# Performance work log

Measured on AMD Instinct MI355X. Metric: run time of the kernel, lower is better.

The kernel has to match this reference:

```python
import jax, jax.numpy as jnp
import numpy as np

HIDDEN = 2048
NUM_HEADS = 16
HEAD_DIM = HIDDEN // NUM_HEADS  # 128
LATENT = HIDDEN // 8            # 256
ROPE_THETA = 100000.0


def setup_inputs() -> dict:
    key = jax.random.key(0)
    ks = jax.random.split(key, 7)
    s = 0.02
    x = jax.random.normal(ks[0], (4, 1024, HIDDEN), dtype=jnp.float32)
    # weights stored as [in, out] (transpose of torch nn.Linear.weight)
    w_q_down = jax.random.normal(ks[1], (HIDDEN, LATENT), dtype=jnp.float32) * s
    w_kv_down = jax.random.normal(ks[2], (HIDDEN, LATENT), dtype=jnp.float32) * s
    w_q_up = jax.random.normal(ks[3], (LATENT, HIDDEN), dtype=jnp.float32) * s
    w_k_up = jax.random.normal(ks[4], (LATENT, HIDDEN), dtype=jnp.float32) * s
    w_v_up = jax.random.normal(ks[5], (LATENT, HIDDEN), dtype=jnp.float32) * s
    w_o = jax.random.normal(ks[6], (HIDDEN, HIDDEN), dtype=jnp.float32) * s
    return {"x": x, "w_q_down": w_q_down, "w_kv_down": w_kv_down,
            "w_q_up": w_q_up, "w_k_up": w_k_up, "w_v_up": w_v_up, "w_o": w_o}


def _rope_cos_sin(seq_len, dtype):
    # Llama rotary: inv_freq over even dims, emb = concat(freqs, freqs)
    inv_freq = 1.0 / (ROPE_THETA ** (jnp.arange(0, HEAD_DIM, 2, dtype=jnp.float32) / HEAD_DIM))
    pos = jnp.arange(seq_len, dtype=jnp.float32)
    freqs = pos[:, None] * inv_freq[None, :]          # [S, D/2]
    emb = jnp.concatenate([freqs, freqs], axis=-1)    # [S, D]
    return jnp.cos(emb).astype(dtype), jnp.sin(emb).astype(dtype)


def _rotate_half(t):
    h = t.shape[-1] // 2
    return jnp.concatenate([-t[..., h:], t[..., :h]], axis=-1)


def reference(x, w_q_down, w_kv_down, w_q_up, w_k_up, w_v_up, w_o):
    B, S, H = x.shape
    q_latent = x @ w_q_down                 # [B,S,latent]
    kv_latent = x @ w_kv_down               # [B,S,latent]
    q = (q_latent @ w_q_up).reshape(B, S, NUM_HEADS, HEAD_DIM)
    k = (kv_latent @ w_k_up).reshape(B, S, NUM_HEADS, HEAD_DIM)
    v = (kv_latent @ w_v_up).reshape(B, S, NUM_HEADS, HEAD_DIM)

    cos, sin = _rope_cos_sin(S, x.dtype)    # [S,D]
    cos = cos[None, :, None, :]             # [1,S,1,D] (unsqueeze_dim=2)
    sin = sin[None, :, None, :]
    q = q * cos + _rotate_half(q) * sin
    k = k * cos + _rotate_half(k) * sin

    # [B,H,S,D]
    q = q.transpose(0, 2, 1, 3)
    k = k.transpose(0, 2, 1, 3)
    v = v.transpose(0, 2, 1, 3)

    scale = 1.0 / jnp.sqrt(jnp.asarray(HEAD_DIM, dtype=x.dtype))
    scores = jnp.einsum('bhqd,bhkd->bhqk', q, k) * scale
    causal = jnp.tril(jnp.ones((S, S), dtype=bool))
    scores = jnp.where(causal[None, None], scores, jnp.finfo(scores.dtype).min)
    probs = jax.nn.softmax(scores, axis=-1)
    attn = jnp.einsum('bhqk,bhkd->bhqd', probs, v)  # [B,H,S,D]
    attn = attn.transpose(0, 2, 1, 3).reshape(B, S, H)
    return attn @ w_o
```

## Files before the change

kernel.cpp:

```cpp
#include <hip/hip_runtime.h>
#include <hip/hip_bf16.h>

typedef unsigned short u16;
typedef unsigned int u32;
typedef __attribute__((ext_vector_type(8))) __bf16 bf16x8;
typedef __attribute__((ext_vector_type(4))) float f32x4;

#define HID 2048
#define NH 16
#define HD 128
#define LAT 256
#define BATCH 4
#define SEQ 1024

__device__ __forceinline__ u16 f2bf(float f) {
  union { float f; u32 u; } v; v.f = f;
  u32 r = v.u + 0x7fffu + ((v.u >> 16) & 1u);
  return (u16)(r >> 16);
}

typedef const __attribute__((address_space(1))) u32 as1_u32;
typedef __attribute__((address_space(3))) u32 as3_u32;

__device__ __forceinline__ void load_lds16(const void* g, void* l) {
  __builtin_amdgcn_global_load_lds((as1_u32*)g, (as3_u32*)l, 16, 0, 0);
}

template<int WM, int WN, int MR, int NR>
__device__ __forceinline__ void gemm_core(const u16* __restrict__ A, const u16* __restrict__ Bt,
    int K, int lda, int ldb, int arow0, int brow0, u16* As, u16* Bs, f32x4 acc[MR][NR]) {
  constexpr int BM = WM * MR * 16, BN = WN * NR * 16;
  constexpr int NW = WM * WN;
  constexpr int ACH = (BM * 32) / 512;
  constexpr int BCH = (BN * 32) / 512;
  const int tid = threadIdx.x;
  const int lane = tid & 63, wave = tid >> 6;
  const int wm = wave % WM, wn = wave / WM;
  const int fr = lane & 15, fq = lane >> 4;

  for (int kt = 0; kt < K; kt += 32) {
    __syncthreads();
    #pragma unroll
    for (int cc = 0; cc < ACH / NW; ++cc) {
      int c = wave + cc * NW;
      int r = c * 16 + (lane >> 2);
      int col = (lane & 3) * 8;
      load_lds16(&A[(size_t)(arow0 + r) * lda + kt + col], &As[c * 512]);
    }
    #pragma unroll
    for (int cc = 0; cc < BCH / NW; ++cc) {
      int c = wave + cc * NW;
      int r = c * 16 + (lane >> 2);
      int col = (lane & 3) * 8;
      load_lds16(&Bt[(size_t)(brow0 + r) * ldb + kt + col], &Bs[c * 512]);
    }
    asm volatile("s_waitcnt vmcnt(0)" ::: "memory");
    __syncthreads();
    bf16x8 af[MR], bfr[NR];
    #pragma unroll
    for (int m = 0; m < MR; ++m)
      af[m] = *(const bf16x8*)&As[(wm * MR * 16 + m * 16 + fr) * 32 + fq * 8];
    #pragma unroll
    for (int n = 0; n < NR; ++n)
      bfr[n] = *(const bf16x8*)&Bs[(wn * NR * 16 + n * 16 + fr) * 32 + fq * 8];
    #pragma unroll
    for (int m = 0; m < MR; ++m)
      #pragma unroll
      for (int n = 0; n < NR; ++n)
        acc[m][n] = __builtin_amdgcn_mfma_f32_16x16x32_bf16(af[m], bfr[n], acc[m][n], 0, 0, 0);
  }
}

__global__ void __launch_bounds__(256) k_cvt(const float* __restrict__ in, u16* __restrict__ o, int n4) {
  int i = blockIdx.x * blockDim.x + threadIdx.x;
  if (i < n4) {
    float4 v = ((const float4*)in)[i];
    union { u16 s[4]; uint2 u; } w;
    w.s[0] = f2bf(v.x); w.s[1] = f2bf(v.y); w.s[2] = f2bf(v.z); w.s[3] = f2bf(v.w);
    ((uint2*)o)[i] = w.u;
  }
}

__global__ void __launch_bounds__(256) k_transpose3(const float* __restrict__ in0,
    const float* __restrict__ in1, const float* __restrict__ in2,
    u16* __restrict__ o0, u16* __restrict__ o1, u16* __restrict__ o2, int R, int C) {
  __shared__ float t[32][33];
  const float* in = blockIdx.z == 0 ? in0 : (blockIdx.z == 1 ? in1 : in2);
  u16* o = blockIdx.z == 0 ? o0 : (blockIdx.z == 1 ? o1 : o2);
  int bx = blockIdx.x * 32, by = blockIdx.y * 32;
  int tx = threadIdx.x, ty = threadIdx.y;
  #pragma unroll
  for (int i = ty; i < 32; i += 8) t[i][tx] = in[(size_t)(by + i) * C + bx + tx];
  __syncthreads();
  #pragma unroll
  for (int i = ty; i < 32; i += 8) o[(size_t)(bx + i) * R + by + tx] = f2bf(t[tx][i]);
}

__global__ void __launch_bounds__(256) k_cossin(float* __restrict__ cosT, float* __restrict__ sinT) {
  int idx = blockIdx.x * 256 + threadIdx.x;
  int s = idx >> 6, d = idx & 63;
  float inv = powf(100000.0f, -(float)d / 64.0f);
  float a = (float)s * inv;
  cosT[idx] = cosf(a);
  sinT[idx] = sinf(a);
}

__global__ void __launch_bounds__(512, 2) k_down(const u16* __restrict__ xb, const u16* __restrict__ wqdT,
    const u16* __restrict__ wkvdT, u16* __restrict__ ql, u16* __restrict__ kvl) {
  __shared__ __align__(16) u16 As[2][128 * 128];
  __shared__ __align__(16) u16 Bs[2][64 * 128];
  const u16* Bt = blockIdx.z ? wkvdT : wqdT;
  u16* out = blockIdx.z ? kvl : ql;
  const int rb = blockIdx.x * 128, cb = blockIdx.y * 64;
  const int tid = threadIdx.x, lane = tid & 63, wave = tid >> 6;
  const int wm = wave & 3, wn = wave >> 2;
  const int fr = lane & 15, fq = lane >> 4;
  const char* Ab = (const char*)xb;
  const char* Bb = (const char*)Bt;
  f32x4 acc[2][2] = {};

  auto stage = [&](int buf, int s) {
    #pragma unroll
    for (int cc = 0; cc < 4; ++cc) {
      int c = wave * 4 + cc;
      int L = c * 1024 + lane * 16;
      int Ls = L ^ (((L >> 8) & 7) << 4);
      int r = Ls >> 8, colb = Ls & 255;
      load_lds16(Ab + (size_t)(rb + r) * 4096 + s * 256 + colb, (char*)As[buf] + c * 1024);
    }
    #pragma unroll
    for (int cc = 0; cc < 2; ++cc) {
      int c = wave * 2 + cc;
      int L = c * 1024 + lane * 16;
      int Ls = L ^ (((L >> 8) & 7) << 4);
      int r = Ls >> 8, colb = Ls & 255;
      load_lds16(Bb + (size_t)(cb + r) * 4096 + s * 256 + colb, (char*)Bs[buf] + c * 1024);
    }
  };

  stage(0, 0);
  int buf = 0;
  for (int s = 0; s < 16; ++s) {
    if (s + 1 < 16) {
      stage(buf ^ 1, s + 1);
      asm volatile("s_waitcnt vmcnt(6)" ::: "memory");
    } else {
      asm volatile("s_waitcnt vmcnt(0)" ::: "memory");
    }
    asm volatile("s_barrier" ::: "memory");

    #pragma unroll
    for (int kk = 0; kk < 4; ++kk) {
      bf16x8 af[2], bfr[2];
      #pragma unroll
      for (int m = 0; m < 2; ++m) {
        int r = wm * 32 + m * 16 + fr;
        af[m] = *(const bf16x8*)((const char*)As[buf] + ((r * 256 + kk * 64 + fq * 16) ^ ((r & 7) << 4)));
      }
      #pragma unroll
      for (int n = 0; n < 2; ++n) {
        int r = wn * 32 + n * 16 + fr;
        bfr[n] = *(const bf16x8*)((const char*)Bs[buf] + ((r * 256 + kk * 64 + fq * 16) ^ ((r & 7) << 4)));
      }
      #pragma unroll
      for (int m = 0; m < 2; ++m)
        #pragma unroll
        for (int n = 0; n < 2; ++n)
          acc[m][n] = __builtin_amdgcn_mfma_f32_16x16x32_bf16(af[m], bfr[n], acc[m][n], 0, 0, 0);
    }

    asm volatile("s_barrier" ::: "memory");
    buf ^= 1;
  }

  #pragma unroll
  for (int m = 0; m < 2; ++m)
    #pragma unroll
    for (int n = 0; n < 2; ++n)
      #pragma unroll
      for (int i = 0; i < 4; ++i)
        out[(size_t)(rb + wm * 32 + m * 16 + fq * 4 + i) * LAT + cb + wn * 32 + n * 16 + fr] =
            f2bf(acc[m][n][i]);
}

__global__ void __launch_bounds__(256) k_up(const u16* __restrict__ ql, const u16* __restrict__ kvl,
    const u16* __restrict__ wquT, const u16* __restrict__ wkuT, const u16* __restrict__ wvuT,
    u16* __restrict__ q, u16* __restrict__ k, u16* __restrict__ vt,
    const float* __restrict__ cosT, const float* __restrict__ sinT) {
  __shared__ __align__(16) u16 As[128 * 32];
  __shared__ __align__(16) u16 Bs[128 * 32];
  const int mode = blockIdx.z;
  const u16* A = (mode == 0) ? ql : kvl;
  const u16* Bt = (mode == 0) ? wquT : (mode == 1 ? wkuT : wvuT);
  const int rb = blockIdx.x * 128;
  const int h = blockIdx.y;
  f32x4 acc[2][8] = {};
  gemm_core<4, 1, 2, 8>(A, Bt, LAT, LAT, LAT, rb, h * HD, As, Bs, acc);
  const int lane = threadIdx.x & 63, wave = threadIdx.x >> 6;
  const int fr = lane & 15, fq = lane >> 4;
  if (mode == 2) {
    #pragma unroll
    for (int m = 0; m < 2; ++m)
      #pragma unroll
      for (int n = 0; n < 8; ++n)
        #pragma unroll
        for (int i = 0; i < 4; ++i) {
          int row = rb + wave * 32 + m * 16 + fq * 4 + i;
          int b = row >> 10, s = row & 1023;
          int sp = (s & ~63) | (((s >> 4) & 1) << 5) | (((s >> 3) & 1) << 4) |
                   (((s >> 2) & 1) << 3) | (((s >> 5) & 1) << 2) | (s & 3);
          vt[(size_t)((b * NH + h) * HD + n * 16 + fr) * SEQ + sp] = f2bf(acc[m][n][i]);
        }
  } else {
    u16* dst = (mode == 0) ? q : k;
    const float scale = (mode == 0) ? 0.08838834764831845f * 1.4426950408889634f : 1.0f;
    #pragma unroll
    for (int m = 0; m < 2; ++m)
      #pragma unroll
      for (int i = 0; i < 4; ++i) {
        int row = rb + wave * 32 + m * 16 + fq * 4 + i;
        int b = row >> 10, s = row & 1023;
        size_t base = (size_t)((b * NH + h) * SEQ + s) * HD;
        #pragma unroll
        for (int j = 0; j < 4; ++j) {
          int dlo = j * 16 + fr;
          float c = cosT[s * 64 + dlo], sn = sinT[s * 64 + dlo];
          float x1 = acc[m][j][i], x2 = acc[m][j + 4][i];
          dst[base + dlo] = f2bf((x1 * c - x2 * sn) * scale);
          dst[base + dlo + 64] = f2bf((x2 * c + x1 * sn) * scale);
        }
      }
  }
}

__global__ void __launch_bounds__(1024, 1) k_attn(const u16* __restrict__ Q, const u16* __restrict__ Kc,
    const u16* __restrict__ Vt, u16* __restrict__ O) {
  __shared__ __align__(16) u16 Ks[2][64 * 128];
  __shared__ __align__(16) u16 Vs[2][128 * 64];
  const int f = blockIdx.x;
  const int bh = (f & 7) * 8 + ((f >> 3) & 7);
  const int jp = f >> 6;
  const int jh = 7 - jp, jl = jp;
  const int h = bh & (NH - 1), b = bh >> 4;
  const int tid = threadIdx.x, lane = tid & 63, wave = tid >> 6;
  const int fr = lane & 15, fq = lane >> 4;
  const int qw = ((wave < 8) ? jh : jl) * 128 + (wave & 7) * 16;
  const size_t qkb = (size_t)bh * SEQ * HD;
  const char* Kbase = (const char*)Kc + qkb * 2;
  const char* Vbase = (const char*)Vt + (size_t)bh * HD * SEQ * 2;
  const int nkt = 2 * jh + 2;

  auto stage = [&](int buf, int kt) {
    int c = wave;
    int L = c * 1024 + lane * 16;
    int Lk = L ^ (((L >> 8) & 7) << 4);
    load_lds16(Kbase + (size_t)kt * 16384 + Lk, (char*)Ks[buf] + c * 1024);
    int Lv = L ^ (((L >> 7) & 7) << 4);
    int rv = Lv >> 7, colb = Lv & 127;
    load_lds16(Vbase + (size_t)rv * (SEQ * 2) + (size_t)kt * 128 + colb, (char*)Vs[buf] + c * 1024);
  };

  bf16x8 ones;
  #pragma unroll
  for (int z = 0; z < 8; ++z) ones[z] = (__bf16)1.0f;

  bf16x8 qf[4];
  #pragma unroll
  for (int c = 0; c < 4; ++c)
    qf[c] = *(const bf16x8*)&Q[qkb + (size_t)(qw + fr) * HD + c * 32 + fq * 8];

  f32x4 ao[8] = {};
  f32x4 lacc = {};

  stage(0, 0);

  int cur = 0;
  for (int t = 0; t < nkt; ++t) {
    if (t + 1 < nkt) {
      stage(cur ^ 1, t + 1);
      asm volatile("s_waitcnt vmcnt(2)" ::: "memory");
    } else {
      asm volatile("s_waitcnt vmcnt(0)" ::: "memory");
    }
    asm volatile("s_barrier" ::: "memory");

    const int k0 = t * 64;
    if (k0 <= qw + 15) {
      f32x4 sc[4] = {};
      __builtin_amdgcn_s_setprio(1);
      #pragma unroll
      for (int c = 0; c < 4; ++c)
        #pragma unroll
        for (int n = 0; n < 4; ++n) {
          int rr = n * 16 + fr;
          int off = (rr * 256 + c * 64 + fq * 16) ^ ((rr & 7) << 4);
          bf16x8 kf = *(const bf16x8*)((const char*)Ks[cur] + off);
          sc[n] = __builtin_amdgcn_mfma_f32_16x16x32_bf16(kf, qf[c], sc[n], 0, 0, 0);
        }
      __builtin_amdgcn_s_setprio(0);

      const bool needmask = (k0 + 63 > qw);
      const int qrow = qw + fr;
      float p[4][4];
      #pragma unroll
      for (int n = 0; n < 4; ++n)
        #pragma unroll
        for (int i = 0; i < 4; ++i) {
          float sv = sc[n][i];
          if (needmask) {
            int kg = k0 + n * 16 + fq * 4 + i;
            sv = (kg <= qrow) ? sv : -1e30f;
          }
          p[n][i] = exp2f(sv);
        }
      bf16x8 pa[2];
      #pragma unroll
      for (int kf = 0; kf < 2; ++kf) {
        union { bf16x8 v; u32 w[4]; } pu;
        asm("v_cvt_pk_bf16_f32 %0, %1, %2" : "=v"(pu.w[0]) : "v"(p[kf][0]), "v"(p[kf][1]));
        asm("v_cvt_pk_bf16_f32 %0, %1, %2" : "=v"(pu.w[1]) : "v"(p[kf][2]), "v"(p[kf][3]));
        asm("v_cvt_pk_bf16_f32 %0, %1, %2" : "=v"(pu.w[2]) : "v"(p[2 + kf][0]), "v"(p[2 + kf][1]));
        asm("v_cvt_pk_bf16_f32 %0, %1, %2" : "=v"(pu.w[3]) : "v"(p[2 + kf][2]), "v"(p[2 + kf][3]));
        pa[kf] = pu.v;
      }

      __builtin_amdgcn_s_setprio(1);
      lacc = __builtin_amdgcn_mfma_f32_16x16x32_bf16(pa[0], ones, lacc, 0, 0, 0);
      lacc = __builtin_amdgcn_mfma_f32_16x16x32_bf16(pa[1], ones, lacc, 0, 0, 0);
      #pragma unroll
      for (int jj = 0; jj < 8; ++jj)
        #pragma unroll
        for (int kf = 0; kf < 2; ++kf) {
          int rv = jj * 16 + fr;
          int off = (rv * 128 + kf * 64 + fq * 16) ^ ((rv & 7) << 4);
          bf16x8 vf = *(const bf16x8*)((const char*)Vs[cur] + off);
          ao[jj] = __builtin_amdgcn_mfma_f32_16x16x32_bf16(pa[kf], vf, ao[jj], 0, 0, 0);
        }
      __builtin_amdgcn_s_setprio(0);
    }
    asm volatile("s_barrier" ::: "memory");
    cur ^= 1;
  }

  #pragma unroll
  for (int i = 0; i < 4; ++i) {
    float inv = 1.f / lacc[i];
    int s = qw + fq * 4 + i;
    size_t base = (size_t)(b * SEQ + s) * HID + h * HD;
    #pragma unroll
    for (int jj = 0; jj < 8; ++jj)
      O[base + jj * 16 + fr] = f2bf(ao[jj][i] * inv);
  }
}

__global__ void __launch_bounds__(256) k_out(const u16* __restrict__ at, const u16* __restrict__ woT,
    float* __restrict__ out) {
  __shared__ __align__(16) u16 As[128 * 128];
  __shared__ __align__(16) u16 Bs[128 * 128];
  const int rb = blockIdx.x * 128, cb = blockIdx.y * 128;
  const int tid = threadIdx.x, lane = tid & 63, wave = tid >> 6;
  const int wm = wave & 1, wn = wave >> 1;
  const int fr = lane & 15, fq = lane >> 4;
  const char* Ab = (const char*)at;
  const char* Bb = (const char*)woT;

  f32x4 acc[4][4] = {};

  for (int kt = 0; kt < HID; kt += 128) {
    __syncthreads();
    #pragma unroll
    for (int cc = 0; cc < 8; ++cc) {
      int c = wave * 8 + cc;
      int L = c * 1024 + lane * 16;
      int Ls = L ^ (((L >> 8) & 7) << 4);
      int r = Ls >> 8, colb = Ls & 255;
      load_lds16(Ab + (size_t)(rb + r) * (HID * 2) + kt * 2 + colb, (char*)As + c * 1024);
      load_lds16(Bb + (size_t)(cb + r) * (HID * 2) + kt * 2 + colb, (char*)Bs + c * 1024);
    }
    asm volatile("s_waitcnt vmcnt(0)" ::: "memory");
    __syncthreads();

    #pragma unroll
    for (int kk = 0; kk < 4; ++kk) {
      bf16x8 af[4], bfr[4];
      #pragma unroll
      for (int m = 0; m < 4; ++m) {
        int r = wm * 64 + m * 16 + fr;
        af[m] = *(const bf16x8*)((const char*)As + ((r * 256 + kk * 64 + fq * 16) ^ ((r & 7) << 4)));
      }
      #pragma unroll
      for (int n = 0; n < 4; ++n) {
        int r = wn * 64 + n * 16 + fr;
        bfr[n] = *(const bf16x8*)((const char*)Bs + ((r * 256 + kk * 64 + fq * 16) ^ ((r & 7) << 4)));
      }
      #pragma unroll
      for (int m = 0; m < 4; ++m)
        #pragma unroll
        for (int n = 0; n < 4; ++n)
          acc[m][n] = __builtin_amdgcn_mfma_f32_16x16x32_bf16(af[m], bfr[n], acc[m][n], 0, 0, 0);
    }
  }

  #pragma unroll
  for (int m = 0; m < 4; ++m)
    #pragma unroll
    for (int n = 0; n < 4; ++n)
      #pragma unroll
      for (int i = 0; i < 4; ++i)
        out[(size_t)(rb + wm * 64 + m * 16 + fq * 4 + i) * HID + cb + wn * 64 + n * 16 + fr] =
            acc[m][n][i];
}

extern "C" void kernel_launch(void* const* d_in, const int* in_sizes, int n_in,
                              void* d_out, int out_size, void* d_ws, size_t ws_size,
                              hipStream_t stream) {
  const float* x    = (const float*)d_in[0];
  const float* wqd  = (const float*)d_in[1];
  const float* wkvd = (const float*)d_in[2];
  const float* wqu  = (const float*)d_in[3];
  const float* wku  = (const float*)d_in[4];
  const float* wvu  = (const float*)d_in[5];
  const float* wo   = (const float*)d_in[6];
  float* out = (float*)d_out;

  char* p = (char*)d_ws;
  u16* xb    = (u16*)(p + 0);
  u16* at    = xb;
  u16* wqdT  = (u16*)(p + 16777216);
  u16* wkvdT = (u16*)(p + 17825792);
  u16* wquT  = (u16*)(p + 18874368);
  u16* wkuT  = (u16*)(p + 19922944);
  u16* wvuT  = (u16*)(p + 20971520);
  u16* woT   = (u16*)(p + 22020096);
  u16* ql    = (u16*)(p + 30408704);
  u16* kvl   = (u16*)(p + 32505856);
  u16* q     = (u16*)(p + 34603008);
  u16* kk    = (u16*)(p + 51380224);
  u16* vt    = (u16*)(p + 68157440);
  float* cosT = (float*)(p + 84934656);
  float* sinT = (float*)(p + 85196800);

  k_cvt<<<8192, 256, 0, stream>>>(x, xb, 2097152);
  k_transpose3<<<dim3(8, 64, 2), dim3(32, 8), 0, stream>>>(wqd, wkvd, wkvd, wqdT, wkvdT, wkvdT, 2048, 256);
  k_transpose3<<<dim3(64, 8, 3), dim3(32, 8), 0, stream>>>(wqu, wku, wvu, wquT, wkuT, wvuT, 256, 2048);
  k_transpose3<<<dim3(64, 64, 1), dim3(32, 8), 0, stream>>>(wo, wo, wo, woT, woT, woT, 2048, 2048);
  k_cossin<<<256, 256, 0, stream>>>(cosT, sinT);

  k_down<<<dim3(32, 4, 2), 512, 0, stream>>>(xb, wqdT, wkvdT, ql, kvl);
  k_up<<<dim3(32, 16, 3), 256, 0, stream>>>(ql, kvl, wquT, wkuT, wvuT, q, kk, vt, cosT, sinT);
  k_attn<<<256, 1024, 0, stream>>>(q, kk, vt, at);
  k_out<<<dim3(32, 16), 256, 0, stream>>>(at, woT, out);
}
```

Baseline: 151.2 us.

## Merge preprocessing kernels into one launch and halve k_out K-tile

Folds the x conversion, the three weight-transpose launches and the cos/sin table kernel into a single k_prep kernel that dispatches on block index, cutting five launches down to one. Separately, k_out's K tile shrinks from 128 to 64, which halves its LDS use so more blocks can run per CU, at the cost of twice as many load/barrier iterations. The swizzle is adjusted to match 128-byte rows.

```diff
diff --git a/kernel.cpp b/kernel.cpp
--- a/kernel.cpp
+++ b/kernel.cpp
@@ -71,38 +71,53 @@
   }
 }
 
-__global__ void __launch_bounds__(256) k_cvt(const float* __restrict__ in, u16* __restrict__ o, int n4) {
-  int i = blockIdx.x * blockDim.x + threadIdx.x;
-  if (i < n4) {
-    float4 v = ((const float4*)in)[i];
+__device__ __forceinline__ void prep_transpose(const float* __restrict__ in, u16* __restrict__ o,
+                                               int R, int C, int bxi, int byi, int tid) {
+  __shared__ float t[32][33];
+  int bx = bxi * 32, by = byi * 32;
+  int tx = tid & 31, ty = tid >> 5;
+  #pragma unroll
+  for (int i = ty; i < 32; i += 8) t[i][tx] = in[(size_t)(by + i) * C + bx + tx];
+  __syncthreads();
+  #pragma unroll
+  for (int i = ty; i < 32; i += 8) o[(size_t)(bx + i) * R + by + tx] = f2bf(t[tx][i]);
+}
+
+__global__ void __launch_bounds__(256) k_prep(const float* __restrict__ x, u16* __restrict__ xb,
+    const float* __restrict__ wqd, const float* __restrict__ wkvd,
+    const float* __restrict__ wqu, const float* __restrict__ wku, const float* __restrict__ wvu,
+    const float* __restrict__ wo,
+    u16* __restrict__ wqdT, u16* __restrict__ wkvdT,
+    u16* __restrict__ wquT, u16* __restrict__ wkuT, u16* __restrict__ wvuT,
+    u16* __restrict__ woT, float* __restrict__ cosT, float* __restrict__ sinT) {
+  const int bb = blockIdx.x, tid = threadIdx.x;
+  if (bb < 8192) {
+    int i = bb * 256 + tid;
+    float4 v = ((const float4*)x)[i];
     union { u16 s[4]; uint2 u; } w;
     w.s[0] = f2bf(v.x); w.s[1] = f2bf(v.y); w.s[2] = f2bf(v.z); w.s[3] = f2bf(v.w);
-    ((uint2*)o)[i] = w.u;
-  }
-}
-
-__global__ void __launch_bounds__(256) k_transpose3(const float* __restrict__ in0,
-    const float* __restrict__ in1, const float* __restrict__ in2,
-    u16* __restrict__ o0, u16* __restrict__ o1, u16* __restrict__ o2, int R, int C) {
-  __shared__ float t[32][33];
-  const float* in = blockIdx.z == 0 ? in0 : (blockIdx.z == 1 ? in1 : in2);
-  u16* o = blockIdx.z == 0 ? o0 : (blockIdx.z == 1 ? o1 : o2);
-  int bx = blockIdx.x * 32, by = blockIdx.y * 32;
-  int tx = threadIdx.x, ty = threadIdx.y;
-  #pragma unroll
-  for (int i = ty; i < 32; i += 8) t[i][tx] = in[(size_t)(by + i) * C + bx + tx];
-  __syncthreads();
-  #pragma unroll
-  for (int i = ty; i < 32; i += 8) o[(size_t)(bx + i) * R + by + tx] = f2bf(t[tx][i]);
-}
-
-__global__ void __launch_bounds__(256) k_cossin(float* __restrict__ cosT, float* __restrict__ sinT) {
-  int idx = blockIdx.x * 256 + threadIdx.x;
-  int s = idx >> 6, d = idx & 63;
-  float inv = powf(100000.0f, -(float)d / 64.0f);
-  float a = (float)s * inv;
-  cosT[idx] = cosf(a);
-  sinT[idx] = sinf(a);
+    ((uint2*)xb)[i] = w.u;
+  } else if (bb < 9216) {
+    int i = bb - 8192;
+    int z = i >> 9, r = i & 511;
+    prep_transpose(z ? wkvd : wqd, z ? wkvdT : wqdT, 2048, 256, r & 7, r >> 3, tid);
+  } else if (bb < 10752) {
+    int i = bb - 9216;
+    int z = i >> 9, r = i & 511;
+    const float* in = (z == 0) ? wqu : (z == 1 ? wku : wvu);
+    u16* o = (z == 0) ? wquT : (z == 1 ? wkuT : wvuT);
+    prep_transpose(in, o, 256, 2048, r & 63, r >> 6, tid);
+  } else if (bb < 14848) {
+    int i = bb - 10752;
+    prep_transpose(wo, woT, 2048, 2048, i & 63, i >> 6, tid);
+  } else {
+    int idx = (bb - 14848) * 256 + tid;
+    int s = idx >> 6, d = idx & 63;
+    float inv = powf(100000.0f, -(float)d / 64.0f);
+    float a = (float)s * inv;
+    cosT[idx] = cosf(a);
+    sinT[idx] = sinf(a);
+  }
 }
 
 __global__ void __launch_bounds__(512, 2) k_down(const u16* __restrict__ xb, const u16* __restrict__ wqdT,
@@ -355,8 +370,8 @@
 
 __global__ void __launch_bounds__(256) k_out(const u16* __restrict__ at, const u16* __restrict__ woT,
     float* __restrict__ out) {
-  __shared__ __align__(16) u16 As[128 * 128];
-  __shared__ __align__(16) u16 Bs[128 * 128];
+  __shared__ __align__(16) u16 As[128 * 64];
+  __shared__ __align__(16) u16 Bs[128 * 64];
   const int rb = blockIdx.x * 128, cb = blockIdx.y * 128;
   const int tid = threadIdx.x, lane = tid & 63, wave = tid >> 6;
   const int wm = wave & 1, wn = wave >> 1;
@@ -366,14 +381,14 @@
 
   f32x4 acc[4][4] = {};
 
-  for (int kt = 0; kt < HID; kt += 128) {
+  for (int kt = 0; kt < HID; kt += 64) {
     __syncthreads();
     #pragma unroll
-    for (int cc = 0; cc < 8; ++cc) {
-      int c = wave * 8 + cc;
+    for (int cc = 0; cc < 4; ++cc) {
+      int c = wave * 4 + cc;
       int L = c * 1024 + lane * 16;
-      int Ls = L ^ (((L >> 8) & 7) << 4);
-      int r = Ls >> 8, colb = Ls & 255;
+      int Ls = L ^ (((L >> 7) & 7) << 4);
+      int r = Ls >> 7, colb = Ls & 127;
       load_lds16(Ab + (size_t)(rb + r) * (HID * 2) + kt * 2 + colb, (char*)As + c * 1024);
       load_lds16(Bb + (size_t)(cb + r) * (HID * 2) + kt * 2 + colb, (char*)Bs + c * 1024);
     }
@@ -381,17 +396,17 @@
     __syncthreads();
 
     #pragma unroll
-    for (int kk = 0; kk < 4; ++kk) {
+    for (int kk = 0; kk < 2; ++kk) {
       bf16x8 af[4], bfr[4];
       #pragma unroll
       for (int m = 0; m < 4; ++m) {
         int r = wm * 64 + m * 16 + fr;
-        af[m] = *(const bf16x8*)((const char*)As + ((r * 256 + kk * 64 + fq * 16) ^ ((r & 7) << 4)));
+        af[m] = *(const bf16x8*)((const char*)As + ((r * 128 + kk * 64 + fq * 16) ^ ((r & 7) << 4)));
       }
       #pragma unroll
       for (int n = 0; n < 4; ++n) {
         int r = wn * 64 + n * 16 + fr;
-        bfr[n] = *(const bf16x8*)((const char*)Bs + ((r * 256 + kk * 64 + fq * 16) ^ ((r & 7) << 4)));
+        bfr[n] = *(const bf16x8*)((const char*)Bs + ((r * 128 + kk * 64 + fq * 16) ^ ((r & 7) << 4)));
       }
       #pragma unroll
       for (int m = 0; m < 4; ++m)
@@ -440,11 +455,8 @@
   float* cosT = (float*)(p + 84934656);
   float* sinT = (float*)(p + 85196800);
 
-  k_cvt<<<8192, 256, 0, stream>>>(x, xb, 2097152);
-  k_transpose3<<<dim3(8, 64, 2), dim3(32, 8), 0, stream>>>(wqd, wkvd, wkvd, wqdT, wkvdT, wkvdT, 2048, 256);
-  k_transpose3<<<dim3(64, 8, 3), dim3(32, 8), 0, stream>>>(wqu, wku, wvu, wquT, wkuT, wvuT, 256, 2048);
-  k_transpose3<<<dim3(64, 64, 1), dim3(32, 8), 0, stream>>>(wo, wo, wo, woT, woT, woT, 2048, 2048);
-  k_cossin<<<256, 256, 0, stream>>>(cosT, sinT);
+  k_prep<<<15104, 256, 0, stream>>>(x, xb, wqd, wkvd, wqu, wku, wvu, wo,
+                                    wqdT, wkvdT, wquT, wkuT, wvuT, woT, cosT, sinT);
 
   k_down<<<dim3(32, 4, 2), 512, 0, stream>>>(xb, wqdT, wkvdT, ql, kvl);
   k_up<<<dim3(32, 16, 3), 256, 0, stream>>>(ql, kvl, wquT, wkuT, wvuT, q, kk, vt, cosT, sinT);
```

New measurement: 150.8 us. Within noise of the previous version (-0.2%).
